# Optimization experiments

Hardware: AMD Instinct MI355X
Metric: run time of the kernel (lower is better)

## Reference

```python
import jax, jax.numpy as jnp
import numpy as np

N0, N1, N2 = 500000, 100000, 20000
E1, E2 = 1600000, 320000
DIN, DH, DOUT = 128, 256, 128
EPS_BN = 1e-5
EPS_NORM = 1e-12


def setup_inputs() -> dict:
    key = jax.random.key(0)
    k = jax.random.split(key, 16)
    s = 0.05
    return {
        "x": jax.random.normal(k[0], (N0, DIN), jnp.float32),
        "src1": jax.random.randint(k[1], (E1,), 0, N0),
        "dst1": jax.random.randint(k[2], (E1,), 0, N1),
        "src2": jax.random.randint(k[3], (E2,), 0, N1),
        "dst2": jax.random.randint(k[4], (E2,), 0, N2),
        "n1": N1,
        "n2": N2,
        "W1_1": jax.random.normal(k[5], (DH, DIN), jnp.float32) * s,
        "W2_1": jax.random.normal(k[6], (DH, DIN), jnp.float32) * s,
        "b2_1": jax.random.normal(k[7], (DH,), jnp.float32) * s,
        "gamma1": jax.random.uniform(k[8], (DH,), jnp.float32, 0.5, 1.5),
        "beta1": jax.random.normal(k[9], (DH,), jnp.float32) * s,
        "mean1": jax.random.normal(k[10], (DH,), jnp.float32) * s,
        "var1": jax.random.uniform(k[11], (DH,), jnp.float32, 0.5, 1.5),
        "W1_2": jax.random.normal(k[12], (DOUT, DH), jnp.float32) * s,
        "W2_2": jax.random.normal(k[13], (DOUT, DH), jnp.float32) * s,
        "b2_2": jax.random.normal(k[14], (DOUT,), jnp.float32) * s,
    }


def _mean_agg(h, src, dst, n_target):
    # torch_sparse.matmul(adj_t, h, reduce='mean'): per-target mean of neighbor rows
    ssum = jax.ops.segment_sum(h[src], dst, num_segments=n_target)
    cnt = jax.ops.segment_sum(jnp.ones(src.shape, h.dtype), dst, num_segments=n_target)
    return ssum / jnp.maximum(cnt, 1.0)[:, None]


def _l2norm(h):
    # F.normalize(h, p=2, dim=1)
    n = jnp.sqrt(jnp.sum(h * h, axis=1, keepdims=True))
    return h / jnp.maximum(n, EPS_NORM)


def reference(x, src1, dst1, src2, dst2, n1, n2,
              W1_1, W2_1, b2_1, gamma1, beta1, mean1, var1,
              W1_2, W2_2, b2_2):
    # --- layer 1: SageConv(in=128, out=256) ---
    h_n = _mean_agg(x, src1, dst1, n1)                 # [n1, DIN]
    h = x[:n1] @ W1_1.T + (h_n @ W2_1.T + b2_1)        # [n1, DH]
    h = _l2norm(h)
    # BatchNorm1d (eval mode: running stats), then ReLU; dropout is identity in eval
    h = gamma1 * (h - mean1) * jax.lax.rsqrt(var1 + EPS_BN) + beta1
    h = jax.nn.relu(h)
    # --- layer 2: SageConv(in=256, out=128) ---
    h_n2 = _mean_agg(h, src2, dst2, n2)                # [n2, DH]
    out = h[:n2] @ W1_2.T + (h_n2 @ W2_2.T + b2_2)     # [n2, DOUT]
    return _l2norm(out)
```

## Files before the change

### kernel.cpp

```cpp
#include <hip/hip_runtime.h>
#include <hip/hip_bf16.h>

#define N1C  100000
#define N2C  20000
#define DIN_ 128
#define DH_  256
#define DOUT_ 128
#define CAP_LOG2 6
#define CAP_     64

#define BIN_SHIFT 7
#define NBIN1 782
#define NBIN2 157
#define NBINS 939
#define CAP_BIN 3072
#define CHUNK_A 4096

typedef unsigned short ushort_t;
typedef unsigned int   uint_t;
typedef __attribute__((ext_vector_type(8))) short bf16x8;
typedef __attribute__((ext_vector_type(4))) float f32x4;

__device__ __forceinline__ float bf2f(ushort_t u) {
    return __uint_as_float(((uint_t)u) << 16);
}
__device__ __forceinline__ ushort_t f2bf(float f) {
    uint_t x = __float_as_uint(f);
    x += 0x7fffu + ((x >> 16) & 1u);
    return (ushort_t)(x >> 16);
}

__global__ __launch_bounds__(256) void convert_and_bin_kernel(
    const float* __restrict__ xsrc, ushort_t* __restrict__ xdst, long long n8,
    const float* __restrict__ w0, const float* __restrict__ w1,
    const float* __restrict__ w2, const float* __restrict__ w3,
    ushort_t* __restrict__ wdst,
    const int* __restrict__ src1, const int* __restrict__ dst1, int E1,
    const int* __restrict__ src2, const int* __restrict__ dst2, int E2,
    int* __restrict__ gTail, uint2* __restrict__ binBuf, int nbA)
{
    __shared__ int hist[NBINS];
    __shared__ int binOff[NBINS];
    __shared__ int runc[NBINS];
    __shared__ int gb[NBINS];
    __shared__ uint2 stage[CHUNK_A];
    __shared__ int wtot[4];

    const int tid = threadIdx.x;

    if ((int)blockIdx.x >= nbA) {
        const long long t = (long long)((int)blockIdx.x - nbA) * 256 + tid;
        if (t < n8) {
            const float4 v0 = *(const float4*)(xsrc + t * 8);
            const float4 v1 = *(const float4*)(xsrc + t * 8 + 4);
            uint4 o;
            o.x = (uint_t)f2bf(v0.x) | ((uint_t)f2bf(v0.y) << 16);
            o.y = (uint_t)f2bf(v0.z) | ((uint_t)f2bf(v0.w) << 16);
            o.z = (uint_t)f2bf(v1.x) | ((uint_t)f2bf(v1.y) << 16);
            o.w = (uint_t)f2bf(v1.z) | ((uint_t)f2bf(v1.w) << 16);
            *(uint4*)(xdst + t * 8) = o;
        } else {
            const long long t2 = t - n8;
            if (t2 >= 16384) return;
            const int mat = (int)(t2 >> 12);
            const long long idx = (long long)(t2 & 4095) * 8;
            const float* s = (mat == 0) ? w0 : (mat == 1) ? w1 : (mat == 2) ? w2 : w3;
            const float4 v0 = *(const float4*)(s + idx);
            const float4 v1 = *(const float4*)(s + idx + 4);
            uint4 o;
            o.x = (uint_t)f2bf(v0.x) | ((uint_t)f2bf(v0.y) << 16);
            o.y = (uint_t)f2bf(v0.z) | ((uint_t)f2bf(v0.w) << 16);
            o.z = (uint_t)f2bf(v1.x) | ((uint_t)f2bf(v1.y) << 16);
            o.w = (uint_t)f2bf(v1.z) | ((uint_t)f2bf(v1.w) << 16);
            *(uint4*)(wdst + (long long)mat * 32768 + idx) = o;
        }
        return;
    }

    const int tE = E1 + E2;
    const int c0 = blockIdx.x * CHUNK_A;
    const int cend = (c0 + CHUNK_A < tE) ? (c0 + CHUNK_A) : tE;
    const int ccnt = cend - c0;

    for (int b = tid; b < NBINS; b += 256) hist[b] = 0;
    __syncthreads();

    for (int i = c0 + tid; i < cend; i += 256) {
        int d, bin;
        if (i < E1) { d = dst1[i];      bin = d >> BIN_SHIFT; }
        else        { d = dst2[i - E1]; bin = NBIN1 + (d >> BIN_SHIFT); }
        atomicAdd(&hist[bin], 1);
    }
    __syncthreads();

    {
        int h[4]; int tsum = 0;
        #pragma unroll
        for (int k = 0; k < 4; ++k) {
            const int b = tid * 4 + k;
            h[k] = (b < NBINS) ? hist[b] : 0;
            tsum += h[k];
        }
        int s = tsum;
        #pragma unroll
        for (int o = 1; o < 64; o <<= 1) {
            int t = __shfl_up(s, (unsigned)o);
            if ((tid & 63) >= o) s += t;
        }
        if ((tid & 63) == 63) wtot[tid >> 6] = s;
        __syncthreads();
        int wpre = 0;
        #pragma unroll
        for (int k = 0; k < 4; ++k) wpre += (k < (tid >> 6)) ? wtot[k] : 0;
        int run = wpre + (s - tsum);
        #pragma unroll
        for (int k = 0; k < 4; ++k) {
            const int b = tid * 4 + k;
            if (b < NBINS) {
                binOff[b] = run;
                runc[b]   = run;
                gb[b] = h[k] ? atomicAdd(&gTail[b], h[k]) : 0;
            }
            run += h[k];
        }
    }
    __syncthreads();

    for (int i = c0 + tid; i < cend; i += 256) {
        int s, d, bin;
        if (i < E1) { s = src1[i];      d = dst1[i];      bin = d >> BIN_SHIFT; }
        else        { s = src2[i - E1]; d = dst2[i - E1]; bin = NBIN1 + (d >> BIN_SHIFT); }
        const int r = atomicAdd(&runc[bin], 1);
        stage[r] = make_uint2((uint_t)s, (uint_t)d | ((uint_t)bin << 17));
    }
    __syncthreads();

    for (int i = tid; i < ccnt; i += 256) {
        const uint2 u = stage[i];
        const int bin = (int)(u.y >> 17);
        const int local = gb[bin] + (i - binOff[bin]);
        if (local < CAP_BIN)
            binBuf[(size_t)bin * CAP_BIN + local] = u;
    }
}

__global__ __launch_bounds__(512) void gather1_bucket_kernel(
    const ushort_t* __restrict__ X, const int* __restrict__ gTail,
    const uint2* __restrict__ binBuf, ushort_t* __restrict__ agg)
{
    __shared__ int run[64];
    __shared__ int eLDS[64 * CAP_];

    const int tid = threadIdx.x;
    const int g0 = blockIdx.x << 6;
    const int bin = g0 >> BIN_SHIFT;
    const int half = (g0 >> 6) & 1;
    const int t0 = gTail[bin];
    const int nE = (t0 < CAP_BIN) ? t0 : CAP_BIN;

    if (tid < 64) run[tid] = 0;
    __syncthreads();

    const uint2* bp = binBuf + (size_t)bin * CAP_BIN;
    for (int i = tid; i < nE; i += 512) {
        const uint2 u = bp[i];
        const int ld = (int)(u.y & 127u);
        if ((ld >> 6) == half) {
            const int l = ld & 63;
            const int slot = atomicAdd(&run[l], 1);
            if (slot < CAP_) eLDS[(l << CAP_LOG2) + slot] = (int)u.x;
        }
    }
    __syncthreads();

    const int wid = tid >> 6, lane = tid & 63;
    const int c = lane << 1;
    #pragma unroll
    for (int rr = 0; rr < 8; ++rr) {
        const int l = (wid << 3) + rr;
        const int d = g0 + l;
        if (d >= N1C) break;
        const int deg = run[l];
        const int end = (deg < CAP_) ? deg : CAP_;
        const int* ep = &eLDS[l << CAP_LOG2];
        float ax = 0.f, ay = 0.f;
        int e = 0;
        for (; e + 3 < end; e += 4) {
            const int s0 = ep[e], s1 = ep[e+1], s2 = ep[e+2], s3 = ep[e+3];
            const uint_t u0 = *(const uint_t*)(X + (size_t)s0 * DIN_ + c);
            const uint_t u1 = *(const uint_t*)(X + (size_t)s1 * DIN_ + c);
            const uint_t u2 = *(const uint_t*)(X + (size_t)s2 * DIN_ + c);
            const uint_t u3 = *(const uint_t*)(X + (size_t)s3 * DIN_ + c);
            ax += bf2f((ushort_t)u0) + bf2f((ushort_t)u1)
                + bf2f((ushort_t)u2) + bf2f((ushort_t)u3);
            ay += bf2f((ushort_t)(u0 >> 16)) + bf2f((ushort_t)(u1 >> 16))
                + bf2f((ushort_t)(u2 >> 16)) + bf2f((ushort_t)(u3 >> 16));
        }
        for (; e < end; ++e) {
            const uint_t u0 = *(const uint_t*)(X + (size_t)ep[e] * DIN_ + c);
            ax += bf2f((ushort_t)u0);
            ay += bf2f((ushort_t)(u0 >> 16));
        }
        const float r = 1.0f / fmaxf((float)deg, 1.0f);
        const uint_t o = (uint_t)f2bf(ax * r) | ((uint_t)f2bf(ay * r) << 16);
        *(uint_t*)(agg + (size_t)d * DIN_ + c) = o;
    }
}

__global__ __launch_bounds__(512) void gather2_bucket_kernel(
    const ushort_t* __restrict__ X, const int* __restrict__ gTail,
    const uint2* __restrict__ binBuf, ushort_t* __restrict__ agg)
{
    __shared__ int run[64];
    __shared__ int eLDS[64 * CAP_];

    const int tid = threadIdx.x;
    const int g0 = blockIdx.x << 6;
    const int bin = NBIN1 + (g0 >> BIN_SHIFT);
    const int half = (g0 >> 6) & 1;
    const int t0 = gTail[bin];
    const int nE = (t0 < CAP_BIN) ? t0 : CAP_BIN;

    if (tid < 64) run[tid] = 0;
    __syncthreads();

    const uint2* bp = binBuf + (size_t)bin * CAP_BIN;
    for (int i = tid; i < nE; i += 512) {
        const uint2 u = bp[i];
        const int ld = (int)(u.y & 127u);
        if ((ld >> 6) == half) {
            const int l = ld & 63;
            const int slot = atomicAdd(&run[l], 1);
            if (slot < CAP_) eLDS[(l << CAP_LOG2) + slot] = (int)u.x;
        }
    }
    __syncthreads();

    const int wid = tid >> 6, lane = tid & 63;
    const int c = lane << 2;
    #pragma unroll
    for (int rr = 0; rr < 8; ++rr) {
        const int l = (wid << 3) + rr;
        const int d = g0 + l;
        if (d >= N2C) break;
        const int deg = run[l];
        const int end = (deg < CAP_) ? deg : CAP_;
        const int* ep = &eLDS[l << CAP_LOG2];
        float a0 = 0.f, a1 = 0.f, a2 = 0.f, a3 = 0.f;
        int e = 0;
        for (; e + 3 < end; e += 4) {
            const int s0 = ep[e], s1 = ep[e+1], s2 = ep[e+2], s3 = ep[e+3];
            const uint2 u0 = *(const uint2*)(X + (size_t)s0 * DH_ + c);
            const uint2 u1 = *(const uint2*)(X + (size_t)s1 * DH_ + c);
            const uint2 u2 = *(const uint2*)(X + (size_t)s2 * DH_ + c);
            const uint2 u3 = *(const uint2*)(X + (size_t)s3 * DH_ + c);
            a0 += bf2f((ushort_t)u0.x) + bf2f((ushort_t)u1.x)
                + bf2f((ushort_t)u2.x) + bf2f((ushort_t)u3.x);
            a1 += bf2f((ushort_t)(u0.x >> 16)) + bf2f((ushort_t)(u1.x >> 16))
                + bf2f((ushort_t)(u2.x >> 16)) + bf2f((ushort_t)(u3.x >> 16));
            a2 += bf2f((ushort_t)u0.y) + bf2f((ushort_t)u1.y)
                + bf2f((ushort_t)u2.y) + bf2f((ushort_t)u3.y);
            a3 += bf2f((ushort_t)(u0.y >> 16)) + bf2f((ushort_t)(u1.y >> 16))
                + bf2f((ushort_t)(u2.y >> 16)) + bf2f((ushort_t)(u3.y >> 16));
        }
        for (; e < end; ++e) {
            const uint2 u0 = *(const uint2*)(X + (size_t)ep[e] * DH_ + c);
            a0 += bf2f((ushort_t)u0.x);
            a1 += bf2f((ushort_t)(u0.x >> 16));
            a2 += bf2f((ushort_t)u0.y);
            a3 += bf2f((ushort_t)(u0.y >> 16));
        }
        const float r = 1.0f / fmaxf((float)deg, 1.0f);
        uint2 o;
        o.x = (uint_t)f2bf(a0 * r) | ((uint_t)f2bf(a1 * r) << 16);
        o.y = (uint_t)f2bf(a2 * r) | ((uint_t)f2bf(a3 * r) << 16);
        *(uint2*)(agg + (size_t)d * DH_ + c) = o;
    }
}

__global__ __launch_bounds__(256) void gemm1_fused(
    const ushort_t* __restrict__ A1, const ushort_t* __restrict__ B1,
    const ushort_t* __restrict__ A2, const ushort_t* __restrict__ B2,
    const float* __restrict__ bias,
    const float* __restrict__ gamma, const float* __restrict__ beta,
    const float* __restrict__ mean, const float* __restrict__ var,
    ushort_t* __restrict__ H, int M)
{
    __shared__ ushort_t As[64][40];
    __shared__ ushort_t Bs[256][40];
    __shared__ float rowss[4][64];

    const int tid = threadIdx.x;
    const int m0 = blockIdx.x * 64;

    const int ar = tid >> 2;
    const int aq = (tid & 3) * 8;
    const bool arow_ok = (m0 + ar) < M;

    const int wid  = tid >> 6;
    const int lane = tid & 63;
    const int lm   = lane & 15;
    const int lqq  = lane >> 4;
    const int wcol = wid * 64;

    const f32x4 fzero = {0.f, 0.f, 0.f, 0.f};
    f32x4 acc[4][4];
    #pragma unroll
    for (int i = 0; i < 4; ++i)
        #pragma unroll
        for (int j = 0; j < 4; ++j) acc[i][j] = fzero;

    #pragma unroll
    for (int phase = 0; phase < 2; ++phase) {
        const ushort_t* __restrict__ A = phase ? A2 : A1;
        const ushort_t* __restrict__ B = phase ? B2 : B1;
        const ushort_t* Ap = A + (size_t)(m0 + ar) * 128 + aq;
        const ushort_t* Bp = B + (size_t)tid * 128;

        #pragma unroll
        for (int k0 = 0; k0 < 128; k0 += 32) {
            uint4 a = {0, 0, 0, 0};
            if (arow_ok) a = *(const uint4*)(Ap + k0);
            const uint4 b0 = *(const uint4*)(Bp + k0);
            const uint4 b1 = *(const uint4*)(Bp + k0 + 8);
            const uint4 b2 = *(const uint4*)(Bp + k0 + 16);
            const uint4 b3 = *(const uint4*)(Bp + k0 + 24);

            __syncthreads();
            *(uint4*)&As[ar][aq]   = a;
            *(uint4*)&Bs[tid][0]   = b0;
            *(uint4*)&Bs[tid][8]   = b1;
            *(uint4*)&Bs[tid][16]  = b2;
            *(uint4*)&Bs[tid][24]  = b3;
            __syncthreads();

            bf16x8 af[4], bfr[4];
            #pragma unroll
            for (int i = 0; i < 4; ++i)
                af[i] = *(const bf16x8*)&As[i * 16 + lm][lqq * 8];
            #pragma unroll
            for (int j = 0; j < 4; ++j)
                bfr[j] = *(const bf16x8*)&Bs[wcol + j * 16 + lm][lqq * 8];

            #pragma unroll
            for (int i = 0; i < 4; ++i)
                #pragma unroll
                for (int j = 0; j < 4; ++j)
                    acc[i][j] = __builtin_amdgcn_mfma_f32_16x16x32_bf16(
                        af[i], bfr[j], acc[i][j], 0, 0, 0);
        }
    }

    float bj[4], sc[4], sh[4];
    #pragma unroll
    for (int j = 0; j < 4; ++j) {
        const int C = wcol + j * 16 + lm;
        bj[j] = bias[C];
        const float is = rsqrtf(var[C] + 1e-5f);
        sc[j] = gamma[C] * is;
        sh[j] = beta[C] - mean[C] * gamma[C] * is;
    }

    float ss[4][4];
    #pragma unroll
    for (int i = 0; i < 4; ++i) {
        #pragma unroll
        for (int r = 0; r < 4; ++r) {
            float s = 0.f;
            #pragma unroll
            for (int j = 0; j < 4; ++j) {
                const float v = acc[i][j][r] + bj[j];
                acc[i][j][r] = v;
                s += v * v;
            }
            s += __shfl_xor(s, 1);
            s += __shfl_xor(s, 2);
            s += __shfl_xor(s, 4);
            s += __shfl_xor(s, 8);
            ss[i][r] = s;
        }
    }
    if (lm == 0) {
        #pragma unroll
        for (int i = 0; i < 4; ++i)
            #pragma unroll
            for (int r = 0; r < 4; ++r)
                rowss[wid][i * 16 + lqq * 4 + r] = ss[i][r];
    }
    __syncthreads();

    #pragma unroll
    for (int i = 0; i < 4; ++i) {
        #pragma unroll
        for (int r = 0; r < 4; ++r) {
            const int R = i * 16 + lqq * 4 + r;
            const float tot = rowss[0][R] + rowss[1][R] + rowss[2][R] + rowss[3][R];
            const float inv = 1.0f / fmaxf(sqrtf(tot), 1e-12f);
            const int row = m0 + R;
            if (row < M) {
                const size_t base = (size_t)row * DH_ + wcol + lm;
                #pragma unroll
                for (int j = 0; j < 4; ++j) {
                    const float v = fmaxf(acc[i][j][r] * inv * sc[j] + sh[j], 0.f);
                    H[base + j * 16] = f2bf(v);
                }
            }
        }
    }
}

__global__ __launch_bounds__(256) void gemm2_fused(
    const ushort_t* __restrict__ A1, const ushort_t* __restrict__ B1,
    const ushort_t* __restrict__ A2, const ushort_t* __restrict__ B2,
    const float* __restrict__ bias,
    float* __restrict__ Cout, int M)
{
    __shared__ ushort_t As[128][40];
    __shared__ ushort_t Bs[128][40];
    __shared__ float rowss[2][128];

    const int tid = threadIdx.x;
    const int m0 = blockIdx.x * 128;

    const int lr = tid >> 1;
    const int lq = (tid & 1) * 8;

    const int wid  = tid >> 6;
    const int lane = tid & 63;
    const int lm   = lane & 15;
    const int lqq  = lane >> 4;
    const int wrow = (wid >> 1) * 64;
    const int wcol = (wid & 1) * 64;
    const int wc   = wid & 1;

    const f32x4 fzero = {0.f, 0.f, 0.f, 0.f};
    f32x4 acc[4][4];
    #pragma unroll
    for (int i = 0; i < 4; ++i)
        #pragma unroll
        for (int j = 0; j < 4; ++j) acc[i][j] = fzero;

    const bool arow_ok = (m0 + lr) < M;

    #pragma unroll
    for (int phase = 0; phase < 2; ++phase) {
        const ushort_t* __restrict__ A = phase ? A2 : A1;
        const ushort_t* __restrict__ B = phase ? B2 : B1;
        const ushort_t* Ap = A + (size_t)(m0 + lr) * 256 + lq;
        const ushort_t* Bp = B + (size_t)lr * 256 + lq;

        for (int k0 = 0; k0 < 256; k0 += 32) {
            uint4 a0 = {0, 0, 0, 0}, a1 = {0, 0, 0, 0};
            if (arow_ok) {
                a0 = *(const uint4*)(Ap + k0);
                a1 = *(const uint4*)(Ap + k0 + 16);
            }
            const uint4 b0 = *(const uint4*)(Bp + k0);
            const uint4 b1 = *(const uint4*)(Bp + k0 + 16);

            __syncthreads();
            *(uint4*)&As[lr][lq]      = a0;
            *(uint4*)&As[lr][lq + 16] = a1;
            *(uint4*)&Bs[lr][lq]      = b0;
            *(uint4*)&Bs[lr][lq + 16] = b1;
            __syncthreads();

            bf16x8 af[4], bfr[4];
            #pragma unroll
            for (int i = 0; i < 4; ++i)
                af[i] = *(const bf16x8*)&As[wrow + i * 16 + lm][lqq * 8];
            #pragma unroll
            for (int j = 0; j < 4; ++j)
                bfr[j] = *(const bf16x8*)&Bs[wcol + j * 16 + lm][lqq * 8];

            #pragma unroll
            for (int i = 0; i < 4; ++i)
                #pragma unroll
                for (int j = 0; j < 4; ++j)
                    acc[i][j] = __builtin_amdgcn_mfma_f32_16x16x32_bf16(
                        af[i], bfr[j], acc[i][j], 0, 0, 0);
        }
    }

    float bj[4];
    #pragma unroll
    for (int j = 0; j < 4; ++j) bj[j] = bias[wcol + j * 16 + lm];

    float ss[4][4];
    #pragma unroll
    for (int i = 0; i < 4; ++i) {
        #pragma unroll
        for (int r = 0; r < 4; ++r) {
            float s = 0.f;
            #pragma unroll
            for (int j = 0; j < 4; ++j) {
                const float v = acc[i][j][r] + bj[j];
                acc[i][j][r] = v;
                s += v * v;
            }
            s += __shfl_xor(s, 1);
            s += __shfl_xor(s, 2);
            s += __shfl_xor(s, 4);
            s += __shfl_xor(s, 8);
            ss[i][r] = s;
        }
    }
    if (lm == 0) {
        #pragma unroll
        for (int i = 0; i < 4; ++i)
            #pragma unroll
            for (int r = 0; r < 4; ++r)
                rowss[wc][wrow + i * 16 + lqq * 4 + r] = ss[i][r];
    }
    __syncthreads();

    #pragma unroll
    for (int i = 0; i < 4; ++i) {
        #pragma unroll
        for (int r = 0; r < 4; ++r) {
            const int R = wrow + i * 16 + lqq * 4 + r;
            const float tot = rowss[0][R] + rowss[1][R];
            const float inv = 1.0f / fmaxf(sqrtf(tot), 1e-12f);
            const int row = m0 + R;
            if (row < M) {
                const size_t base = (size_t)row * DOUT_ + wcol + lm;
                #pragma unroll
                for (int j = 0; j < 4; ++j)
                    Cout[base + j * 16] = acc[i][j][r] * inv;
            }
        }
    }
}

extern "C" void kernel_launch(void* const* d_in, const int* in_sizes, int n_in,
                              void* d_out, int out_size, void* d_ws, size_t ws_size,
                              hipStream_t stream)
{
    const float* x     = (const float*)d_in[0];
    const int*   src1  = (const int*)d_in[1];
    const int*   dst1  = (const int*)d_in[2];
    const int*   src2  = (const int*)d_in[3];
    const int*   dst2  = (const int*)d_in[4];
    const float* W1_1  = (const float*)d_in[7];
    const float* W2_1  = (const float*)d_in[8];
    const float* b2_1  = (const float*)d_in[9];
    const float* gamma1= (const float*)d_in[10];
    const float* beta1 = (const float*)d_in[11];
    const float* mean1 = (const float*)d_in[12];
    const float* var1  = (const float*)d_in[13];
    const float* W1_2  = (const float*)d_in[14];
    const float* W2_2  = (const float*)d_in[15];
    const float* b2_2  = (const float*)d_in[16];
    float* out = (float*)d_out;

    const int E1 = in_sizes[1];
    const int E2 = in_sizes[3];
    const int n1 = N1C;
    const int n2 = N2C;

    char* wsb = (char*)d_ws;
    ushort_t* xb     = (ushort_t*)(wsb + 0);
    ushort_t* h      = (ushort_t*)(wsb + 128000000);
    ushort_t* agg1   = (ushort_t*)(wsb + 179200000);
    ushort_t* agg2   = (ushort_t*)(wsb + 204800000);
    ushort_t* wb     = (ushort_t*)(wsb + 215040000);
    int*      gTail  = (int*)(wsb + 215302144);
    uint2*    binBuf = (uint2*)(wsb + 215306240);
    ushort_t* w11b = wb;
    ushort_t* w21b = wb + 32768;
    ushort_t* w12b = wb + 65536;
    ushort_t* w22b = wb + 98304;

    hipMemsetAsync(gTail, 0, NBINS * sizeof(int), stream);
    {
        const long long n8 = (long long)500000 * DIN_ / 8;
        const int tE = E1 + E2;
        const int nbA = (tE + CHUNK_A - 1) / CHUNK_A;
        const int nblk = nbA + (int)(n8 / 256) + 64;
        convert_and_bin_kernel<<<nblk, 256, 0, stream>>>(
            x, xb, n8, W1_1, W2_1, W1_2, W2_2, wb,
            src1, dst1, E1, src2, dst2, E2, gTail, binBuf, nbA);
    }

    gather1_bucket_kernel<<<(n1 + 63) / 64, 512, 0, stream>>>(xb, gTail, binBuf, agg1);
    gemm1_fused<<<(n1 + 63) / 64, 256, 0, stream>>>(
        xb, w11b, agg1, w21b, b2_1, gamma1, beta1, mean1, var1, h, n1);

    gather2_bucket_kernel<<<(n2 + 63) / 64, 512, 0, stream>>>(h, gTail, binBuf, agg2);
    gemm2_fused<<<(n2 + 127) / 128, 256, 0, stream>>>(
        h, w12b, agg2, w22b, b2_2, out, n2);
}
```

Baseline: 604.2 us.

## Fuse layer-1 neighbor gather into GEMM1 via shared-memory aggregate tile

Merges the layer-1 bucketed mean aggregation into the GEMM1 kernel. Each 64-row block now gathers its neighbor means into an LDS tile and feeds that tile straight to the second MFMA phase, so the agg1 buffer is never written to or read back from global memory and one kernel launch goes away. The trade-off is a larger LDS footprint (about 45KB with eLDS and aggLDS) and 256 threads instead of 512 doing the gather. Both may lower occupancy and the latency hiding for the random row reads.

```diff
diff --git a/kernel.cpp b/kernel.cpp
--- a/kernel.cpp
+++ b/kernel.cpp
@@ -144,66 +144,220 @@
     }
 }
 
-__global__ __launch_bounds__(512) void gather1_bucket_kernel(
-    const ushort_t* __restrict__ X, const int* __restrict__ gTail,
-    const uint2* __restrict__ binBuf, ushort_t* __restrict__ agg)
+__global__ __launch_bounds__(256) void gemm1_gather_fused(
+    const ushort_t* __restrict__ X, const ushort_t* __restrict__ B1,
+    const ushort_t* __restrict__ B2,
+    const int* __restrict__ gTail, const uint2* __restrict__ binBuf,
+    const float* __restrict__ bias,
+    const float* __restrict__ gamma, const float* __restrict__ beta,
+    const float* __restrict__ mean, const float* __restrict__ var,
+    ushort_t* __restrict__ H, int M)
 {
+    __shared__ ushort_t As[64][40];
+    __shared__ ushort_t Bs[256][40];
+    __shared__ ushort_t aggLDS[64][136];
     __shared__ int run[64];
     __shared__ int eLDS[64 * CAP_];
+    __shared__ float rowss[4][64];
 
     const int tid = threadIdx.x;
-    const int g0 = blockIdx.x << 6;
-    const int bin = g0 >> BIN_SHIFT;
-    const int half = (g0 >> 6) & 1;
-    const int t0 = gTail[bin];
-    const int nE = (t0 < CAP_BIN) ? t0 : CAP_BIN;
+    const int m0 = blockIdx.x * 64;
+    const int bin  = m0 >> BIN_SHIFT;
+    const int half = (m0 >> 6) & 1;
 
     if (tid < 64) run[tid] = 0;
     __syncthreads();
-
-    const uint2* bp = binBuf + (size_t)bin * CAP_BIN;
-    for (int i = tid; i < nE; i += 512) {
-        const uint2 u = bp[i];
-        const int ld = (int)(u.y & 127u);
-        if ((ld >> 6) == half) {
-            const int l = ld & 63;
-            const int slot = atomicAdd(&run[l], 1);
-            if (slot < CAP_) eLDS[(l << CAP_LOG2) + slot] = (int)u.x;
-        }
-    }
-    __syncthreads();
-
-    const int wid = tid >> 6, lane = tid & 63;
-    const int c = lane << 1;
-    #pragma unroll
-    for (int rr = 0; rr < 8; ++rr) {
-        const int l = (wid << 3) + rr;
-        const int d = g0 + l;
-        if (d >= N1C) break;
-        const int deg = run[l];
-        const int end = (deg < CAP_) ? deg : CAP_;
-        const int* ep = &eLDS[l << CAP_LOG2];
-        float ax = 0.f, ay = 0.f;
-        int e = 0;
-        for (; e + 3 < end; e += 4) {
-            const int s0 = ep[e], s1 = ep[e+1], s2 = ep[e+2], s3 = ep[e+3];
-            const uint_t u0 = *(const uint_t*)(X + (size_t)s0 * DIN_ + c);
-            const uint_t u1 = *(const uint_t*)(X + (size_t)s1 * DIN_ + c);
-            const uint_t u2 = *(const uint_t*)(X + (size_t)s2 * DIN_ + c);
-            const uint_t u3 = *(const uint_t*)(X + (size_t)s3 * DIN_ + c);
-            ax += bf2f((ushort_t)u0) + bf2f((ushort_t)u1)
-                + bf2f((ushort_t)u2) + bf2f((ushort_t)u3);
-            ay += bf2f((ushort_t)(u0 >> 16)) + bf2f((ushort_t)(u1 >> 16))
-                + bf2f((ushort_t)(u2 >> 16)) + bf2f((ushort_t)(u3 >> 16));
-        }
-        for (; e < end; ++e) {
-            const uint_t u0 = *(const uint_t*)(X + (size_t)ep[e] * DIN_ + c);
-            ax += bf2f((ushort_t)u0);
-            ay += bf2f((ushort_t)(u0 >> 16));
-        }
-        const float r = 1.0f / fmaxf((float)deg, 1.0f);
-        const uint_t o = (uint_t)f2bf(ax * r) | ((uint_t)f2bf(ay * r) << 16);
-        *(uint_t*)(agg + (size_t)d * DIN_ + c) = o;
+    {
+        const int t0 = gTail[bin];
+        const int nE = (t0 < CAP_BIN) ? t0 : CAP_BIN;
+        const uint2* bp = binBuf + (size_t)bin * CAP_BIN;
+        for (int i = tid; i < nE; i += 256) {
+            const uint2 u = bp[i];
+            const int ld = (int)(u.y & 127u);
+            if ((ld >> 6) == half) {
+                const int l = ld & 63;
+                const int slot = atomicAdd(&run[l], 1);
+                if (slot < CAP_) eLDS[(l << CAP_LOG2) + slot] = (int)u.x;
+            }
+        }
+    }
+    __syncthreads();
+
+    const int wid  = tid >> 6;
+    const int lane = tid & 63;
+
+    {
+        const int c = lane << 1;
+        for (int rr = 0; rr < 16; ++rr) {
+            const int l = wid * 16 + rr;
+            const int deg = run[l];
+            const int end = (deg < CAP_) ? deg : CAP_;
+            const int* ep = &eLDS[l << CAP_LOG2];
+            float ax = 0.f, ay = 0.f;
+            int e = 0;
+            for (; e + 3 < end; e += 4) {
+                const int s0 = ep[e], s1 = ep[e+1], s2 = ep[e+2], s3 = ep[e+3];
+                const uint_t u0 = *(const uint_t*)(X + (size_t)s0 * DIN_ + c);
+                const uint_t u1 = *(const uint_t*)(X + (size_t)s1 * DIN_ + c);
+                const uint_t u2 = *(const uint_t*)(X + (size_t)s2 * DIN_ + c);
+                const uint_t u3 = *(const uint_t*)(X + (size_t)s3 * DIN_ + c);
+                ax += bf2f((ushort_t)u0) + bf2f((ushort_t)u1)
+                    + bf2f((ushort_t)u2) + bf2f((ushort_t)u3);
+                ay += bf2f((ushort_t)(u0 >> 16)) + bf2f((ushort_t)(u1 >> 16))
+                    + bf2f((ushort_t)(u2 >> 16)) + bf2f((ushort_t)(u3 >> 16));
+            }
+            for (; e < end; ++e) {
+                const uint_t u0 = *(const uint_t*)(X + (size_t)ep[e] * DIN_ + c);
+                ax += bf2f((ushort_t)u0);
+                ay += bf2f((ushort_t)(u0 >> 16));
+            }
+            const float r = 1.0f / fmaxf((float)deg, 1.0f);
+            *(uint_t*)&aggLDS[l][c] =
+                (uint_t)f2bf(ax * r) | ((uint_t)f2bf(ay * r) << 16);
+        }
+    }
+    __syncthreads();
+
+    const int ar = tid >> 2;
+    const int aq = (tid & 3) * 8;
+    const bool arow_ok = (m0 + ar) < M;
+
+    const int lm  = lane & 15;
+    const int lqq = lane >> 4;
+    const int wcol = wid * 64;
+
+    const f32x4 fzero = {0.f, 0.f, 0.f, 0.f};
+    f32x4 acc[4][4];
+    #pragma unroll
+    for (int i = 0; i < 4; ++i)
+        #pragma unroll
+        for (int j = 0; j < 4; ++j) acc[i][j] = fzero;
+
+    {
+        const ushort_t* Ap = X + (size_t)(m0 + ar) * 128 + aq;
+        const ushort_t* Bp = B1 + (size_t)tid * 128;
+        #pragma unroll
+        for (int k0 = 0; k0 < 128; k0 += 32) {
+            uint4 a = {0, 0, 0, 0};
+            if (arow_ok) a = *(const uint4*)(Ap + k0);
+            const uint4 b0 = *(const uint4*)(Bp + k0);
+            const uint4 b1 = *(const uint4*)(Bp + k0 + 8);
+            const uint4 b2 = *(const uint4*)(Bp + k0 + 16);
+            const uint4 b3 = *(const uint4*)(Bp + k0 + 24);
+
+            __syncthreads();
+            *(uint4*)&As[ar][aq]   = a;
+            *(uint4*)&Bs[tid][0]   = b0;
+            *(uint4*)&Bs[tid][8]   = b1;
+            *(uint4*)&Bs[tid][16]  = b2;
+            *(uint4*)&Bs[tid][24]  = b3;
+            __syncthreads();
+
+            bf16x8 af[4], bfr[4];
+            #pragma unroll
+            for (int i = 0; i < 4; ++i)
+                af[i] = *(const bf16x8*)&As[i * 16 + lm][lqq * 8];
+            #pragma unroll
+            for (int j = 0; j < 4; ++j)
+                bfr[j] = *(const bf16x8*)&Bs[wcol + j * 16 + lm][lqq * 8];
+
+            #pragma unroll
+            for (int i = 0; i < 4; ++i)
+                #pragma unroll
+                for (int j = 0; j < 4; ++j)
+                    acc[i][j] = __builtin_amdgcn_mfma_f32_16x16x32_bf16(
+                        af[i], bfr[j], acc[i][j], 0, 0, 0);
+        }
+    }
+
+    {
+        const ushort_t* Bp = B2 + (size_t)tid * 128;
+        #pragma unroll
+        for (int k0 = 0; k0 < 128; k0 += 32) {
+            const uint4 b0 = *(const uint4*)(Bp + k0);
+            const uint4 b1 = *(const uint4*)(Bp + k0 + 8);
+            const uint4 b2 = *(const uint4*)(Bp + k0 + 16);
+            const uint4 b3 = *(const uint4*)(Bp + k0 + 24);
+
+            __syncthreads();
+            *(uint4*)&Bs[tid][0]   = b0;
+            *(uint4*)&Bs[tid][8]   = b1;
+            *(uint4*)&Bs[tid][16]  = b2;
+            *(uint4*)&Bs[tid][24]  = b3;
+            __syncthreads();
+
+            bf16x8 af[4], bfr[4];
+            #pragma unroll
+            for (int i = 0; i < 4; ++i)
+                af[i] = *(const bf16x8*)&aggLDS[i * 16 + lm][k0 + lqq * 8];
+            #pragma unroll
+            for (int j = 0; j < 4; ++j)
+                bfr[j] = *(const bf16x8*)&Bs[wcol + j * 16 + lm][lqq * 8];
+
+            #pragma unroll
+            for (int i = 0; i < 4; ++i)
+                #pragma unroll
+                for (int j = 0; j < 4; ++j)
+                    acc[i][j] = __builtin_amdgcn_mfma_f32_16x16x32_bf16(
+                        af[i], bfr[j], acc[i][j], 0, 0, 0);
+        }
+    }
+
+    float bj[4], sc[4], sh[4];
+    #pragma unroll
+    for (int j = 0; j < 4; ++j) {
+        const int C = wcol + j * 16 + lm;
+        bj[j] = bias[C];
+        const float is = rsqrtf(var[C] + 1e-5f);
+        sc[j] = gamma[C] * is;
+        sh[j] = beta[C] - mean[C] * gamma[C] * is;
+    }
+
+    float ss[4][4];
+    #pragma unroll
+    for (int i = 0; i < 4; ++i) {
+        #pragma unroll
+        for (int r = 0; r < 4; ++r) {
+            float s = 0.f;
+            #pragma unroll
+            for (int j = 0; j < 4; ++j) {
+                const float v = acc[i][j][r] + bj[j];
+                acc[i][j][r] = v;
+                s += v * v;
+            }
+            s += __shfl_xor(s, 1);
+            s += __shfl_xor(s, 2);
+            s += __shfl_xor(s, 4);
+            s += __shfl_xor(s, 8);
+            ss[i][r] = s;
+        }
+    }
+    if (lm == 0) {
+        #pragma unroll
+        for (int i = 0; i < 4; ++i)
+            #pragma unroll
+            for (int r = 0; r < 4; ++r)
+                rowss[wid][i * 16 + lqq * 4 + r] = ss[i][r];
+    }
+    __syncthreads();
+
+    #pragma unroll
+    for (int i = 0; i < 4; ++i) {
+        #pragma unroll
+        for (int r = 0; r < 4; ++r) {
+            const int R = i * 16 + lqq * 4 + r;
+            const float tot = rowss[0][R] + rowss[1][R] + rowss[2][R] + rowss[3][R];
+            const float inv = 1.0f / fmaxf(sqrtf(tot), 1e-12f);
+            const int row = m0 + R;
+            if (row < M) {
+                const size_t base = (size_t)row * DH_ + wcol + lm;
+                #pragma unroll
+                for (int j = 0; j < 4; ++j) {
+                    const float v = fmaxf(acc[i][j][r] * inv * sc[j] + sh[j], 0.f);
+                    H[base + j * 16] = f2bf(v);
+                }
+            }
+        }
     }
 }
 
@@ -278,137 +432,6 @@
     }
 }
 
-__global__ __launch_bounds__(256) void gemm1_fused(
-    const ushort_t* __restrict__ A1, const ushort_t* __restrict__ B1,
-    const ushort_t* __restrict__ A2, const ushort_t* __restrict__ B2,
-    const float* __restrict__ bias,
-    const float* __restrict__ gamma, const float* __restrict__ beta,
-    const float* __restrict__ mean, const float* __restrict__ var,
-    ushort_t* __restrict__ H, int M)
-{
-    __shared__ ushort_t As[64][40];
-    __shared__ ushort_t Bs[256][40];
-    __shared__ float rowss[4][64];
-
-    const int tid = threadIdx.x;
-    const int m0 = blockIdx.x * 64;
-
-    const int ar = tid >> 2;
-    const int aq = (tid & 3) * 8;
-    const bool arow_ok = (m0 + ar) < M;
-
-    const int wid  = tid >> 6;
-    const int lane = tid & 63;
-    const int lm   = lane & 15;
-    const int lqq  = lane >> 4;
-    const int wcol = wid * 64;
-
-    const f32x4 fzero = {0.f, 0.f, 0.f, 0.f};
-    f32x4 acc[4][4];
-    #pragma unroll
-    for (int i = 0; i < 4; ++i)
-        #pragma unroll
-        for (int j = 0; j < 4; ++j) acc[i][j] = fzero;
-
-    #pragma unroll
-    for (int phase = 0; phase < 2; ++phase) {
-        const ushort_t* __restrict__ A = phase ? A2 : A1;
-        const ushort_t* __restrict__ B = phase ? B2 : B1;
-        const ushort_t* Ap = A + (size_t)(m0 + ar) * 128 + aq;
-        const ushort_t* Bp = B + (size_t)tid * 128;
-
-        #pragma unroll
-        for (int k0 = 0; k0 < 128; k0 += 32) {
-            uint4 a = {0, 0, 0, 0};
-            if (arow_ok) a = *(const uint4*)(Ap + k0);
-            const uint4 b0 = *(const uint4*)(Bp + k0);
-            const uint4 b1 = *(const uint4*)(Bp + k0 + 8);
-            const uint4 b2 = *(const uint4*)(Bp + k0 + 16);
-            const uint4 b3 = *(const uint4*)(Bp + k0 + 24);
-
-            __syncthreads();
-            *(uint4*)&As[ar][aq]   = a;
-            *(uint4*)&Bs[tid][0]   = b0;
-            *(uint4*)&Bs[tid][8]   = b1;
-            *(uint4*)&Bs[tid][16]  = b2;
-            *(uint4*)&Bs[tid][24]  = b3;
-            __syncthreads();
-
-            bf16x8 af[4], bfr[4];
-            #pragma unroll
-            for (int i = 0; i < 4; ++i)
-                af[i] = *(const bf16x8*)&As[i * 16 + lm][lqq * 8];
-            #pragma unroll
-            for (int j = 0; j < 4; ++j)
-                bfr[j] = *(const bf16x8*)&Bs[wcol + j * 16 + lm][lqq * 8];
-
-            #pragma unroll
-            for (int i = 0; i < 4; ++i)
-                #pragma unroll
-                for (int j = 0; j < 4; ++j)
-                    acc[i][j] = __builtin_amdgcn_mfma_f32_16x16x32_bf16(
-                        af[i], bfr[j], acc[i][j], 0, 0, 0);
-        }
-    }
-
-    float bj[4], sc[4], sh[4];
-    #pragma unroll
-    for (int j = 0; j < 4; ++j) {
-        const int C = wcol + j * 16 + lm;
-        bj[j] = bias[C];
-        const float is = rsqrtf(var[C] + 1e-5f);
-        sc[j] = gamma[C] * is;
-        sh[j] = beta[C] - mean[C] * gamma[C] * is;
-    }
-
-    float ss[4][4];
-    #pragma unroll
-    for (int i = 0; i < 4; ++i) {
-        #pragma unroll
-        for (int r = 0; r < 4; ++r) {
-            float s = 0.f;
-            #pragma unroll
-            for (int j = 0; j < 4; ++j) {
-                const float v = acc[i][j][r] + bj[j];
-                acc[i][j][r] = v;
-                s += v * v;
-            }
-            s += __shfl_xor(s, 1);
-            s += __shfl_xor(s, 2);
-            s += __shfl_xor(s, 4);
-            s += __shfl_xor(s, 8);
-            ss[i][r] = s;
-        }
-    }
-    if (lm == 0) {
-        #pragma unroll
-        for (int i = 0; i < 4; ++i)
-            #pragma unroll
-            for (int r = 0; r < 4; ++r)
-                rowss[wid][i * 16 + lqq * 4 + r] = ss[i][r];
-    }
-    __syncthreads();
-
-    #pragma unroll
-    for (int i = 0; i < 4; ++i) {
-        #pragma unroll
-        for (int r = 0; r < 4; ++r) {
-            const int R = i * 16 + lqq * 4 + r;
-            const float tot = rowss[0][R] + rowss[1][R] + rowss[2][R] + rowss[3][R];
-            const float inv = 1.0f / fmaxf(sqrtf(tot), 1e-12f);
-            const int row = m0 + R;
-            if (row < M) {
-                const size_t base = (size_t)row * DH_ + wcol + lm;
-                #pragma unroll
-                for (int j = 0; j < 4; ++j) {
-                    const float v = fmaxf(acc[i][j][r] * inv * sc[j] + sh[j], 0.f);
-                    H[base + j * 16] = f2bf(v);
-                }
-            }
-        }
-    }
-}
-
 __global__ __launch_bounds__(256) void gemm2_fused(
     const ushort_t* __restrict__ A1, const ushort_t* __restrict__ B1,
     const ushort_t* __restrict__ A2, const ushort_t* __restrict__ B2,
@@ -561,7 +584,6 @@
     char* wsb = (char*)d_ws;
     ushort_t* xb     = (ushort_t*)(wsb + 0);
     ushort_t* h      = (ushort_t*)(wsb + 128000000);
-    ushort_t* agg1   = (ushort_t*)(wsb + 179200000);
     ushort_t* agg2   = (ushort_t*)(wsb + 204800000);
     ushort_t* wb     = (ushort_t*)(wsb + 215040000);
     int*      gTail  = (int*)(wsb + 215302144);
@@ -582,9 +604,9 @@
             src1, dst1, E1, src2, dst2, E2, gTail, binBuf, nbA);
     }
 
-    gather1_bucket_kernel<<<(n1 + 63) / 64, 512, 0, stream>>>(xb, gTail, binBuf, agg1);
-    gemm1_fused<<<(n1 + 63) / 64, 256, 0, stream>>>(
-        xb, w11b, agg1, w21b, b2_1, gamma1, beta1, mean1, var1, h, n1);
+    gemm1_gather_fused<<<(n1 + 63) / 64, 256, 0, stream>>>(
+        xb, w11b, w21b, gTail, binBuf,
+        b2_1, gamma1, beta1, mean1, var1, h, n1);
 
     gather2_bucket_kernel<<<(n2 + 63) / 64, 512, 0, stream>>>(h, gTail, binBuf, agg2);
     gemm2_fused<<<(n2 + 127) / 128, 256, 0, stream>>>(
```

After: 703.0 us. 16.3% more time.
